# Kernel tuning notes

Hardware: AMD Instinct MI355X
Metric: run time of the kernel (lower is better)

Reference implementation:

```python
import jax, jax.numpy as jnp
import numpy as np

EPS = 1e-5
POW = 0.5

def _eig_fun(X, fn):
    # symmetric matrix function via eigendecomposition: V f(diag) V^T
    w, V = jnp.linalg.eigh(X)
    return jnp.einsum('...ij,...j,...kj->...ik', V, fn(w), V)

def sym_pow(X, p):
    return _eig_fun(X, lambda w: jnp.power(w, p))

def sym_log(X):
    return _eig_fun(X, jnp.log)

def sym_exp(X):
    return _eig_fun(X, jnp.exp)

def exp_at(T, G):
    # Riemannian exp of tangent T at base point G (affine-invariant metric)
    Gh = sym_pow(G, 0.5)
    Gnh = sym_pow(G, -0.5)
    return Gh @ sym_exp(Gnh @ T @ Gnh) @ Gh

def bary_geom(X, n_iter=1):
    # Karcher/geodesic mean of batch of SPD matrices X: (B, n, n)
    # init at arithmetic mean, n_iter Karcher flow steps
    G = jnp.mean(X, axis=0)
    for _ in range(n_iter):
        Gh = sym_pow(G, 0.5)
        Gnh = sym_pow(G, -0.5)
        T = jnp.mean(sym_log(Gnh @ X @ Gnh), axis=0)
        G = Gh @ sym_exp(T) @ Gh
    return G

def setup_inputs() -> dict:
    key = jax.random.key(0)
    N, h, n = 256, 16, 64
    k1, k2, k3 = jax.random.split(key, 3)
    A = jax.random.normal(k1, (N, h, n, n), dtype=jnp.float32)
    # well-conditioned SPD inputs with distinct eigenvalues
    X = A @ jnp.swapaxes(A, -1, -2) / n + 0.5 * jnp.eye(n, dtype=jnp.float32)
    Bw = jax.random.normal(k2, (n, n), dtype=jnp.float32) * 0.1
    weight = sym_exp(0.5 * (Bw + Bw.T))  # SPD parameter near identity
    Bm = jax.random.normal(k3, (n, n), dtype=jnp.float32) * 0.1
    M = sym_exp(0.5 * (Bm + Bm.T))       # SPD deformation parameter
    shift = jnp.ones((1,), dtype=jnp.float32)
    return {"X": X, "weight": weight, "M": M, "shift": shift}

def reference(X, weight, M, shift):
    N, h, n, _ = X.shape
    Xb = X.reshape(N * h, n, n)
    Xp = sym_pow(Xb, POW)                  # PowerEig(X, po)
    Mnh = sym_pow(M, -0.5)
    Mh = sym_pow(M, 0.5)
    Xc = Mnh @ Xp @ Mnh                    # CongrG(., M, 'neg')
    Wp = sym_pow(weight, POW)              # PowerEig(weight, po)
    Wc = Mnh @ Wp @ Mnh                    # CongrG1(weight, M, 'neg')

    mean = bary_geom(Xc)                   # BaryGeom (training path)
    mnh = sym_pow(mean, -0.5)
    # pal1(mean, LogG(Xc, mean)) = PT of Riemannian log to identity
    T = sym_log(mnh @ Xc @ mnh)            # (N*h, n, n) tangent at I
    # cal_var: mean squared Riemannian distance to the mean
    var = jnp.mean(jnp.sum(T * T, axis=(-2, -1)))
    T = T * (shift[0] / jnp.sqrt(var + EPS))  # scale1
    Wh = sym_pow(weight, 0.5)
    S = Wh @ T @ Wh                        # pal2(weight, LogG1(.))
    Y = exp_at(S, Wc)                      # ExpG(., weight_deformed)
    Y = Mh @ Y @ Mh                        # CongrG(., M, 'pos')
    Y = sym_pow(Y, 1.0 / POW)              # PowerEig(., 1/po)
    return Y.reshape(N, h, n, n)
```

## Files before the change

### kernel.cpp

```cpp
#include <hip/hip_runtime.h>
#include <math.h>

#define PITCH 72
#define NP 68
#define SW_BATCH 12
#define SW_SMALL 10
#define NPART 32
#define EPS2_ROT 1e-12f

#define OFF_ACCG 0
#define OFF_ACCT (NPART*4096)
#define OFF_BASE (2*NPART*4096)
#define SL_MNH  (OFF_BASE + 0*4096)
#define SL_MH   (OFF_BASE + 1*4096)
#define SL_WH   (OFF_BASE + 2*4096)
#define SL_P    (OFF_BASE + 3*4096)
#define SL_Q    (OFF_BASE + 4*4096)
#define SL_GH   (OFF_BASE + 5*4096)
#define SL_GNH  (OFF_BASE + 6*4096)
#define SL_MNH2 (OFF_BASE + 7*4096)
#define SL_WCH  (OFF_BASE + 8*4096)
#define OFF_VAR (OFF_BASE + 9*4096)
#define SL_SC   (OFF_BASE + 9*4096 + 1)

struct __align__(16) F4 { float v[4]; };

struct __align__(16) Smem {
  float S0[64*PITCH];
  float S1[64*PITCH];
  float w2[64];
  float wc[64];
  float nrm[64];
  float red[256];
  int flag;
};

__device__ __forceinline__ void g2s(float* dst, const float* __restrict__ src) {
  int t = threadIdx.x;
#pragma unroll
  for (int i = 0; i < 4; ++i) {
    int e4 = t + (i << 8);
    F4 vv = *(const F4*)&src[e4 * 4];
    *(F4*)&dst[(e4 >> 4) * PITCH + (e4 & 15) * 4] = vv;
  }
  __syncthreads();
}
__device__ __forceinline__ void s2g(float* __restrict__ dst, const float* src) {
  int t = threadIdx.x;
#pragma unroll
  for (int i = 0; i < 4; ++i) {
    int e4 = t + (i << 8);
    F4 vv = *(const F4*)&src[(e4 >> 4) * PITCH + (e4 & 15) * 4];
    *(F4*)&dst[e4 * 4] = vv;
  }
  __syncthreads();
}

template<int MODE>
__device__ void mmX(Smem& sm) {
  int t = threadIdx.x;
  int R0 = t >> 4;
  int J = (t & 15) * 4;
  float acc[4][4] = {};
  for (int kb = 0; kb < 64; kb += 4) {
    F4 a4[4], b4[4];
#pragma unroll
    for (int i = 0; i < 4; ++i) {
      const float* L = (MODE == 0) ? sm.S1 : sm.S0;
      a4[i] = *(const F4*)&L[(R0 + 16 * i) * PITCH + kb];
    }
#pragma unroll
    for (int kk = 0; kk < 4; ++kk) {
      const float* Rp = (MODE == 0) ? sm.S0 : sm.S1;
      b4[kk] = *(const F4*)&Rp[(kb + kk) * PITCH + J];
    }
#pragma unroll
    for (int i = 0; i < 4; ++i)
#pragma unroll
      for (int kk = 0; kk < 4; ++kk)
#pragma unroll
        for (int m = 0; m < 4; ++m)
          acc[i][m] = fmaf(a4[i].v[kk], b4[kk].v[m], acc[i][m]);
  }
  __syncthreads();
#pragma unroll
  for (int i = 0; i < 4; ++i) {
    F4 o;
#pragma unroll
    for (int m = 0; m < 4; ++m) o.v[m] = acc[i][m];
    *(F4*)&sm.S0[(R0 + 16 * i) * PITCH + J] = o;
  }
  __syncthreads();
}

__device__ void reconT(Smem& sm) {
  __syncthreads();
  int t = threadIdx.x;
  int R0 = t >> 4;
  int J = (t & 15) * 4;
  float acc[4][4] = {};
  for (int k = 0; k < 64; ++k) {
    float w = sm.wc[k];
    float a[4];
#pragma unroll
    for (int i = 0; i < 4; ++i) a[i] = w * sm.S0[k * PITCH + R0 + 16 * i];
    F4 b = *(const F4*)&sm.S0[k * PITCH + J];
#pragma unroll
    for (int i = 0; i < 4; ++i)
#pragma unroll
      for (int m = 0; m < 4; ++m) acc[i][m] = fmaf(a[i], b.v[m], acc[i][m]);
  }
#pragma unroll
  for (int i = 0; i < 4; ++i) {
    F4 o;
#pragma unroll
    for (int m = 0; m < 4; ++m) o.v[m] = acc[i][m];
    *(F4*)&sm.S1[(R0 + 16 * i) * PITCH + J] = o;
  }
  __syncthreads();
}

__device__ float frob2(Smem& sm) {
  int t = threadIdx.x;
  float s = 0.f;
#pragma unroll
  for (int i = 0; i < 4; ++i) {
    int e4 = t + (i << 8);
    F4 vv = *(const F4*)&sm.S0[(e4 >> 4) * PITCH + (e4 & 15) * 4];
#pragma unroll
    for (int m = 0; m < 4; ++m) s = fmaf(vv.v[m], vv.v[m], s);
  }
  sm.red[t] = s;
  __syncthreads();
  for (int o = 128; o; o >>= 1) { if (t < o) sm.red[t] += sm.red[t + o]; __syncthreads(); }
  float f = sm.red[0];
  __syncthreads();
  return f;
}

__device__ void hestenes(Smem& sm, int sweeps) {
  const int t = threadIdx.x;
  const int g = t >> 3;
  const int u = t & 7;
  float* A = sm.S0;
  {
    float sa = 0.f, sb = 0.f;
#pragma unroll
    for (int i = 0; i < 8; ++i) {
      float va = A[g * PITCH + u + 8 * i];
      float vb = A[(g + 32) * PITCH + u + 8 * i];
      sa = fmaf(va, va, sa); sb = fmaf(vb, vb, sb);
    }
    sa += __shfl_xor(sa, 1); sa += __shfl_xor(sa, 2); sa += __shfl_xor(sa, 4);
    sb += __shfl_xor(sb, 1); sb += __shfl_xor(sb, 2); sb += __shfl_xor(sb, 4);
    if (u == 0) { sm.nrm[g] = sa; sm.nrm[g + 32] = sb; }
    if (t == 0) sm.flag = 0;
  }
  __syncthreads();

  for (int s = 0; s < sweeps; ++s) {
    for (int r = 0; r < 63; ++r) {
      int p, q;
      if (g == 0) { p = 63; q = r; }
      else {
        int a = r + g;      if (a >= 63) a -= 63;
        int b = r + 63 - g; if (b >= 63) b -= 63;
        p = a; q = b;
      }
      const int bp = p * PITCH + u, bq = q * PITCH + u;
      float cp[8], cq[8];
#pragma unroll
      for (int i = 0; i < 8; ++i) { cp[i] = A[bp + 8 * i]; cq[i] = A[bq + 8 * i]; }
      float d = 0.f;
#pragma unroll
      for (int i = 0; i < 8; ++i) d = fmaf(cp[i], cq[i], d);
      d += __shfl_xor(d, 1); d += __shfl_xor(d, 2); d += __shfl_xor(d, 4);
      float dpp = sm.nrm[p], dqq = sm.nrm[q];
      if (d * d > EPS2_ROT * (dpp * dqq)) {
        float tau = (dqq - dpp) * (0.5f * __builtin_amdgcn_rcpf(d));
        float tt = __builtin_amdgcn_rcpf(fabsf(tau) +
                                         __builtin_amdgcn_sqrtf(fmaf(tau, tau, 1.f)));
        if (tau < 0.f) tt = -tt;
        float c = __builtin_amdgcn_rsqf(fmaf(tt, tt, 1.f));
        float s_ = tt * c;
#pragma unroll
        for (int i = 0; i < 8; ++i) {
          A[bp + 8 * i] = c * cp[i] - s_ * cq[i];
          A[bq + 8 * i] = s_ * cp[i] + c * cq[i];
        }
        if (u == 0) {
          float td = tt * d;
          sm.nrm[p] = dpp - td;
          sm.nrm[q] = dqq + td;
          sm.flag = 1;
        }
      }
      __syncthreads();
    }
    int f = sm.flag;
    __syncthreads();
    if (f == 0) break;
    if (t == 0) sm.flag = 0;
    __syncthreads();
  }

  {
    float sa = 0.f, sb = 0.f;
#pragma unroll
    for (int i = 0; i < 8; ++i) {
      float va = A[g * PITCH + u + 8 * i];
      float vb = A[(g + 32) * PITCH + u + 8 * i];
      sa = fmaf(va, va, sa); sb = fmaf(vb, vb, sb);
    }
    sa += __shfl_xor(sa, 1); sa += __shfl_xor(sa, 2); sa += __shfl_xor(sa, 4);
    sb += __shfl_xor(sb, 1); sb += __shfl_xor(sb, 2); sb += __shfl_xor(sb, 4);
    if (u == 0) { sm.w2[g] = sa; sm.w2[g + 32] = sb; }
  }
  __syncthreads();
}

struct __align__(16) SmemK {
  float A[64*NP];
  float Bop[64*NP];
  float wc[64];
  float red[256];
};
struct __align__(16) SmemK4 {
  float A[64*NP];
  float P[64*NP];
  float Q[64*NP];
  float wc[64];
  float red[256];
};

__device__ __forceinline__ void g2s68(float* dst, const float* __restrict__ src) {
  int t = threadIdx.x;
#pragma unroll
  for (int i = 0; i < 4; ++i) {
    int e4 = t + (i << 8);
    F4 vv = *(const F4*)&src[e4 * 4];
    *(F4*)&dst[(e4 >> 4) * NP + (e4 & 15) * 4] = vv;
  }
  __syncthreads();
}
__device__ __forceinline__ void g2s68s(float* dst, const float* __restrict__ src, float sc) {
  int t = threadIdx.x;
#pragma unroll
  for (int i = 0; i < 4; ++i) {
    int e4 = t + (i << 8);
    F4 vv = *(const F4*)&src[e4 * 4];
#pragma unroll
    for (int m = 0; m < 4; ++m) vv.v[m] *= sc;
    *(F4*)&dst[(e4 >> 4) * NP + (e4 & 15) * 4] = vv;
  }
  __syncthreads();
}

template<int MODE>
__device__ void mm68(float* A, const float* Bo) {
  int t = threadIdx.x;
  int R0 = t >> 4;
  if (MODE == 2) {
    int J0 = t & 15;
    float acc[4][4] = {};
    for (int kb = 0; kb < 64; kb += 4) {
      F4 a4[4];
#pragma unroll
      for (int i = 0; i < 4; ++i) a4[i] = *(const F4*)&A[(R0 + 16 * i) * NP + kb];
#pragma unroll
      for (int kk = 0; kk < 4; ++kk) {
        float b[4];
#pragma unroll
        for (int m = 0; m < 4; ++m) b[m] = Bo[(J0 + 16 * m) * NP + kb + kk];
#pragma unroll
        for (int i = 0; i < 4; ++i)
#pragma unroll
          for (int m = 0; m < 4; ++m) acc[i][m] = fmaf(a4[i].v[kk], b[m], acc[i][m]);
      }
    }
    __syncthreads();
#pragma unroll
    for (int i = 0; i < 4; ++i)
#pragma unroll
      for (int m = 0; m < 4; ++m)
        A[(R0 + 16 * i) * NP + J0 + 16 * m] = acc[i][m];
    __syncthreads();
  } else {
    int J = (t & 15) * 4;
    float acc[4][4] = {};
    for (int kb = 0; kb < 64; kb += 4) {
      F4 a4[4], b4[4];
#pragma unroll
      for (int i = 0; i < 4; ++i) {
        const float* L = (MODE == 0) ? Bo : A;
        a4[i] = *(const F4*)&L[(R0 + 16 * i) * NP + kb];
      }
#pragma unroll
      for (int kk = 0; kk < 4; ++kk) {
        const float* Rp = (MODE == 0) ? A : Bo;
        b4[kk] = *(const F4*)&Rp[(kb + kk) * NP + J];
      }
#pragma unroll
      for (int i = 0; i < 4; ++i)
#pragma unroll
        for (int kk = 0; kk < 4; ++kk)
#pragma unroll
          for (int m = 0; m < 4; ++m)
            acc[i][m] = fmaf(a4[i].v[kk], b4[kk].v[m], acc[i][m]);
    }
    __syncthreads();
#pragma unroll
    for (int i = 0; i < 4; ++i) {
      F4 o;
#pragma unroll
      for (int m = 0; m < 4; ++m) o.v[m] = acc[i][m];
      *(F4*)&A[(R0 + 16 * i) * NP + J] = o;
    }
    __syncthreads();
  }
}

__device__ float frob68(const float* A, float* red) {
  int t = threadIdx.x;
  float s = 0.f;
#pragma unroll
  for (int i = 0; i < 4; ++i) {
    int e4 = t + (i << 8);
    F4 vv = *(const F4*)&A[(e4 >> 4) * NP + (e4 & 15) * 4];
#pragma unroll
    for (int m = 0; m < 4; ++m) s = fmaf(vv.v[m], vv.v[m], s);
  }
  red[t] = s;
  __syncthreads();
  for (int o = 128; o; o >>= 1) { if (t < o) red[t] += red[t + o]; __syncthreads(); }
  float f = red[0];
  __syncthreads();
  return f;
}

__device__ void msq_store(const float* Z, float* __restrict__ gout) {
  int t = threadIdx.x;
  int R0 = t >> 4;
  int J = (t & 15) * 4;
  float acc[4][4] = {};
  for (int kb = 0; kb < 64; kb += 4) {
    F4 a4[4], b4[4];
#pragma unroll
    for (int i = 0; i < 4; ++i) a4[i] = *(const F4*)&Z[(R0 + 16 * i) * NP + kb];
#pragma unroll
    for (int kk = 0; kk < 4; ++kk) b4[kk] = *(const F4*)&Z[(kb + kk) * NP + J];
#pragma unroll
    for (int i = 0; i < 4; ++i)
#pragma unroll
      for (int kk = 0; kk < 4; ++kk)
#pragma unroll
        for (int m = 0; m < 4; ++m)
          acc[i][m] = fmaf(a4[i].v[kk], b4[kk].v[m], acc[i][m]);
  }
#pragma unroll
  for (int i = 0; i < 4; ++i) {
    F4 o;
#pragma unroll
    for (int m = 0; m < 4; ++m) o.v[m] = acc[i][m];
    *(F4*)&gout[(R0 + 16 * i) * 64 + J] = o;
  }
}

__device__ __forceinline__ void hestenes_reg(float (&own)[64], float& w2out, int sweeps) {
  const int lane = threadIdx.x & 63;
  float nrm = 0.f;
#pragma unroll
  for (int i = 0; i < 64; ++i) nrm = fmaf(own[i], own[i], nrm);

  for (int s = 0; s < sweeps; ++s) {
    bool any = false;
    for (int m = 1; m < 64; ++m) {
      float pv[64];
#pragma unroll
      for (int i = 0; i < 64; ++i) pv[i] = __shfl_xor(own[i], m);
      float d0 = 0.f, d1 = 0.f, d2 = 0.f, d3 = 0.f;
#pragma unroll
      for (int i = 0; i < 64; i += 4) {
        d0 = fmaf(own[i + 0], pv[i + 0], d0);
        d1 = fmaf(own[i + 1], pv[i + 1], d1);
        d2 = fmaf(own[i + 2], pv[i + 2], d2);
        d3 = fmaf(own[i + 3], pv[i + 3], d3);
      }
      float d = (d0 + d1) + (d2 + d3);
      float pn = __shfl_xor(nrm, m);
      if (d * d > EPS2_ROT * (nrm * pn)) {
        any = true;
        bool lo = lane < (lane ^ m);
        float dpp = lo ? nrm : pn;
        float dqq = lo ? pn : nrm;
        float tau = (dqq - dpp) * (0.5f * __builtin_amdgcn_rcpf(d));
        float tt = __builtin_amdgcn_rcpf(fabsf(tau) +
                                         __builtin_amdgcn_sqrtf(fmaf(tau, tau, 1.f)));
        if (tau < 0.f) tt = -tt;
        float c = __builtin_amdgcn_rsqf(fmaf(tt, tt, 1.f));
        float s_ = tt * c;
        float sg = lo ? -s_ : s_;
#pragma unroll
        for (int i = 0; i < 64; ++i) own[i] = fmaf(sg, pv[i], c * own[i]);
        float td = tt * d;
        nrm += lo ? -td : td;
      }
    }
    if (!__any((int)any)) break;
  }
  float w = 0.f;
#pragma unroll
  for (int i = 0; i < 64; ++i) w = fmaf(own[i], own[i], w);
  w2out = w;
}


__global__ __launch_bounds__(256) void kzero(float* ws) {
  int i = blockIdx.x * 256 + threadIdx.x;
  if (i < OFF_BASE) ws[i] = 0.f;
  if (i == 0) ws[OFF_VAR] = 0.f;
}

__global__ __launch_bounds__(256, 4) void kprep(const float* __restrict__ weight,
                                                const float* __restrict__ M,
                                                float* ws) {
  __shared__ Smem sm;
  int t = threadIdx.x;
  g2s(sm.S0, M);
  hestenes(sm, SW_SMALL);
  if (t < 64) sm.wc[t] = powf(fmaxf(sm.w2[t], 1e-12f), -1.25f);
  reconT(sm); s2g(ws + SL_MNH, sm.S1);
  if (t < 64) sm.wc[t] = powf(fmaxf(sm.w2[t], 1e-12f), -0.75f);
  reconT(sm); s2g(ws + SL_MH, sm.S1);

  g2s(sm.S0, weight);
  hestenes(sm, SW_SMALL);
  if (t < 64) sm.wc[t] = powf(fmaxf(sm.w2[t], 1e-12f), -0.75f);
  reconT(sm); s2g(ws + SL_WH, sm.S1);

  g2s(sm.S0, ws + SL_MNH);
  mmX<1>(sm);
  g2s(sm.S1, ws + SL_MNH);
  mmX<1>(sm);
  hestenes(sm, SW_SMALL);
  if (t < 64) sm.wc[t] = powf(fmaxf(sm.w2[t], 1e-12f), -0.75f);
  reconT(sm); s2g(ws + SL_WCH, sm.S1);
  if (t < 64) sm.wc[t] = powf(fmaxf(sm.w2[t], 1e-12f), -1.25f);
  reconT(sm);
  g2s(sm.S0, ws + SL_WH);
  mmX<0>(sm);
  s2g(ws + SL_P, sm.S0);
  g2s(sm.S0, ws + SL_WCH);
  g2s(sm.S1, ws + SL_MH);
  mmX<0>(sm);
  s2g(ws + SL_Q, sm.S0);
}

__global__ __launch_bounds__(256, 1) void k1(const float* __restrict__ X,
                                             float* __restrict__ out, float* ws) {
  __shared__ SmemK sm;
  int t = threadIdx.x;
  int w = t >> 6, lane = t & 63;
  size_t b = blockIdx.x;
  g2s68(sm.Bop, ws + SL_MNH);

  float own[64]; float w2;
  {
    const float* Xm = X + (b * 4 + w) * 4096 + (size_t)lane * 64;
#pragma unroll
    for (int j = 0; j < 16; ++j) {
      F4 r = *(const F4*)&Xm[4 * j];
      own[4 * j + 0] = r.v[0]; own[4 * j + 1] = r.v[1];
      own[4 * j + 2] = r.v[2]; own[4 * j + 3] = r.v[3];
    }
  }
  hestenes_reg(own, w2, SW_BATCH);
  __syncthreads();

  int R0 = t >> 4, J = (t & 15) * 4;
  for (int m = 0; m < 4; ++m) {
    if (w == m) {
#pragma unroll
      for (int j = 0; j < 16; ++j) {
        F4 o = {{own[4 * j], own[4 * j + 1], own[4 * j + 2], own[4 * j + 3]}};
        *(F4*)&sm.A[lane * NP + 4 * j] = o;
      }
      sm.wc[lane] = powf(fmaxf(w2, 1e-12f), -0.75f);
    }
    __syncthreads();
    mm68<1>(sm.A, sm.Bop);
    float acc[4][4] = {};
    for (int k = 0; k < 64; ++k) {
      float wck = sm.wc[k];
      float a[4];
#pragma unroll
      for (int i = 0; i < 4; ++i) a[i] = wck * sm.A[k * NP + R0 + 16 * i];
      F4 bb = *(const F4*)&sm.A[k * NP + J];
#pragma unroll
      for (int i = 0; i < 4; ++i)
#pragma unroll
        for (int mc = 0; mc < 4; ++mc) acc[i][mc] = fmaf(a[i], bb.v[mc], acc[i][mc]);
    }
    float* Xc = out + (b * 4 + m) * 4096;
    float* accp = ws + OFF_ACCG + (size_t)((b * 4 + m) & (NPART - 1)) * 4096;
#pragma unroll
    for (int i = 0; i < 4; ++i) {
      F4 o;
#pragma unroll
      for (int mc = 0; mc < 4; ++mc) o.v[mc] = acc[i][mc];
      int base = (R0 + 16 * i) * 64 + J;
      *(F4*)&Xc[base] = o;
#pragma unroll
      for (int mc = 0; mc < 4; ++mc) atomicAdd(accp + base + mc, o.v[mc]);
    }
    __syncthreads();
  }
}

__global__ __launch_bounds__(256, 4) void ksmall2(float* ws, float invB) {
  __shared__ Smem sm;
  int t = threadIdx.x;
#pragma unroll
  for (int i = 0; i < 4; ++i) {
    int e4 = t + (i << 8);
    F4 sum = {{0.f, 0.f, 0.f, 0.f}};
    for (int p = 0; p < NPART; ++p) {
      F4 vv = *(const F4*)&ws[OFF_ACCG + p * 4096 + e4 * 4];
#pragma unroll
      for (int m = 0; m < 4; ++m) sum.v[m] += vv.v[m];
    }
#pragma unroll
    for (int m = 0; m < 4; ++m) sum.v[m] *= invB;
    *(F4*)&sm.S0[(e4 >> 4) * PITCH + (e4 & 15) * 4] = sum;
  }
  __syncthreads();
  hestenes(sm, SW_SMALL);
  if (t < 64) sm.wc[t] = powf(fmaxf(sm.w2[t], 1e-12f), -0.75f);
  reconT(sm); s2g(ws + SL_GH, sm.S1);
  if (t < 64) sm.wc[t] = powf(fmaxf(sm.w2[t], 1e-12f), -1.25f);
  reconT(sm); s2g(ws + SL_GNH, sm.S1);
}

__global__ __launch_bounds__(256, 1) void k2(const float* __restrict__ XcBuf, float* ws) {
  __shared__ SmemK sm;
  int t = threadIdx.x;
  int w = t >> 6, lane = t & 63;
  size_t b = blockIdx.x;
  g2s68(sm.Bop, ws + SL_GNH);

  float own[64]; float w2;
  for (int m = 0; m < 4; ++m) {
    g2s68(sm.A, XcBuf + (b * 4 + m) * 4096);
    mm68<1>(sm.A, sm.Bop);
    mm68<0>(sm.A, sm.Bop);
    if (w == m) {
#pragma unroll
      for (int i = 0; i < 64; ++i) own[i] = sm.A[i * NP + lane];
    }
    __syncthreads();
  }
  hestenes_reg(own, w2, SW_BATCH);
  __syncthreads();

  int R0 = t >> 4, J = (t & 15) * 4;
  for (int m = 0; m < 4; ++m) {
    if (w == m) {
#pragma unroll
      for (int j = 0; j < 16; ++j) {
        F4 o = {{own[4 * j], own[4 * j + 1], own[4 * j + 2], own[4 * j + 3]}};
        *(F4*)&sm.A[lane * NP + 4 * j] = o;
      }
      float s2 = fmaxf(w2, 1e-12f);
      sm.wc[lane] = 0.5f * logf(s2) / s2;
    }
    __syncthreads();
    float acc[4][4] = {};
    for (int k = 0; k < 64; ++k) {
      float wck = sm.wc[k];
      float a[4];
#pragma unroll
      for (int i = 0; i < 4; ++i) a[i] = wck * sm.A[k * NP + R0 + 16 * i];
      F4 bb = *(const F4*)&sm.A[k * NP + J];
#pragma unroll
      for (int i = 0; i < 4; ++i)
#pragma unroll
        for (int mc = 0; mc < 4; ++mc) acc[i][mc] = fmaf(a[i], bb.v[mc], acc[i][mc]);
    }
    float* accp = ws + OFF_ACCT + (size_t)((b * 4 + m) & (NPART - 1)) * 4096;
#pragma unroll
    for (int i = 0; i < 4; ++i) {
      int base = (R0 + 16 * i) * 64 + J;
#pragma unroll
      for (int mc = 0; mc < 4; ++mc) atomicAdd(accp + base + mc, acc[i][mc]);
    }
    __syncthreads();
  }
}

__global__ __launch_bounds__(256, 4) void ksmall3(float* ws, float invB) {
  __shared__ Smem sm;
  int t = threadIdx.x;
#pragma unroll
  for (int i = 0; i < 4; ++i) {
    int e4 = t + (i << 8);
    F4 sum = {{0.f, 0.f, 0.f, 0.f}};
    for (int p = 0; p < NPART; ++p) {
      F4 vv = *(const F4*)&ws[OFF_ACCT + p * 4096 + e4 * 4];
#pragma unroll
      for (int m = 0; m < 4; ++m) sum.v[m] += vv.v[m];
    }
#pragma unroll
    for (int m = 0; m < 4; ++m) sum.v[m] *= invB;
    *(F4*)&sm.S0[(e4 >> 4) * PITCH + (e4 & 15) * 4] = sum;
  }
  __syncthreads();
  float mu = sqrtf(frob2(sm)) + 1e-3f;
  if (t < 64) sm.S0[t * PITCH + t] += mu;
  __syncthreads();
  hestenes(sm, SW_SMALL);
  if (t < 64) {
    float s2 = fmaxf(sm.w2[t], 1e-12f);
    sm.wc[t] = expf(sqrtf(s2) - mu) / s2;
  }
  reconT(sm);
  g2s(sm.S0, ws + SL_GH);
  mmX<1>(sm);
  g2s(sm.S1, ws + SL_GH);
  mmX<1>(sm);
  hestenes(sm, SW_SMALL);
  if (t < 64) sm.wc[t] = powf(fmaxf(sm.w2[t], 1e-12f), -1.25f);
  reconT(sm); s2g(ws + SL_MNH2, sm.S1);
}

__global__ __launch_bounds__(256, 1) void k3(float* __restrict__ buf, float* ws) {
  __shared__ SmemK sm;
  int t = threadIdx.x;
  int w = t >> 6, lane = t & 63;
  size_t b = blockIdx.x;
  g2s68(sm.Bop, ws + SL_MNH2);

  float own[64]; float w2;
  for (int m = 0; m < 4; ++m) {
    g2s68(sm.A, buf + (b * 4 + m) * 4096);
    mm68<1>(sm.A, sm.Bop);
    mm68<0>(sm.A, sm.Bop);
    if (w == m) {
#pragma unroll
      for (int i = 0; i < 64; ++i) own[i] = sm.A[i * NP + lane];
    }
    __syncthreads();
  }
  hestenes_reg(own, w2, SW_BATCH);
  __syncthreads();

  int R0 = t >> 4, J = (t & 15) * 4;
  for (int m = 0; m < 4; ++m) {
    if (w == m) {
#pragma unroll
      for (int j = 0; j < 16; ++j) {
        F4 o = {{own[4 * j], own[4 * j + 1], own[4 * j + 2], own[4 * j + 3]}};
        *(F4*)&sm.A[lane * NP + 4 * j] = o;
      }
      float s2 = fmaxf(w2, 1e-12f);
      sm.wc[lane] = 0.5f * logf(s2) / s2;
    }
    __syncthreads();
    float acc[4][4] = {};
    for (int k = 0; k < 64; ++k) {
      float wck = sm.wc[k];
      float a[4];
#pragma unroll
      for (int i = 0; i < 4; ++i) a[i] = wck * sm.A[k * NP + R0 + 16 * i];
      F4 bb = *(const F4*)&sm.A[k * NP + J];
#pragma unroll
      for (int i = 0; i < 4; ++i)
#pragma unroll
        for (int mc = 0; mc < 4; ++mc) acc[i][mc] = fmaf(a[i], bb.v[mc], acc[i][mc]);
    }
    float* Tg = buf + (b * 4 + m) * 4096;
    float ssq = 0.f;
#pragma unroll
    for (int i = 0; i < 4; ++i) {
      F4 o;
#pragma unroll
      for (int mc = 0; mc < 4; ++mc) o.v[mc] = acc[i][mc];
      int base = (R0 + 16 * i) * 64 + J;
      *(F4*)&Tg[base] = o;
#pragma unroll
      for (int mc = 0; mc < 4; ++mc) ssq = fmaf(o.v[mc], o.v[mc], ssq);
    }
    sm.red[t] = ssq;
    __syncthreads();
    for (int o = 128; o; o >>= 1) { if (t < o) sm.red[t] += sm.red[t + o]; __syncthreads(); }
    if (t == 0) atomicAdd(ws + OFF_VAR, sm.red[0]);
    __syncthreads();
  }
}

__global__ void kscale(float* ws, const float* __restrict__ shift, float invB) {
  if (threadIdx.x == 0 && blockIdx.x == 0) {
    float var = ws[OFF_VAR] * invB;
    ws[SL_SC] = shift[0] / sqrtf(var + 1e-5f);
  }
}

__global__ __launch_bounds__(256, 1) void k4(float* __restrict__ buf, float* ws) {
  __shared__ SmemK4 sm;
  int t = threadIdx.x;
  int w = t >> 6, lane = t & 63;
  size_t b = blockIdx.x;
  float sc = ws[SL_SC];
  g2s68(sm.P, ws + SL_P);
  g2s68(sm.Q, ws + SL_Q);

  float own[64]; float w2; float muw = 0.f;
  for (int m = 0; m < 4; ++m) {
    g2s68s(sm.A, buf + (b * 4 + m) * 4096, sc);
    mm68<0>(sm.A, sm.P);
    mm68<2>(sm.A, sm.P);
    float f = frob68(sm.A, sm.red);
    if (w == m) {
      muw = sqrtf(f) + 1e-3f;
#pragma unroll
      for (int i = 0; i < 64; ++i) {
        float v = sm.A[i * NP + lane];
        own[i] = v + ((i == lane) ? muw : 0.f);
      }
    }
    __syncthreads();
  }
  hestenes_reg(own, w2, SW_BATCH);
  __syncthreads();

  int R0 = t >> 4, J = (t & 15) * 4;
  for (int m = 0; m < 4; ++m) {
    if (w == m) {
#pragma unroll
      for (int j = 0; j < 16; ++j) {
        F4 o = {{own[4 * j], own[4 * j + 1], own[4 * j + 2], own[4 * j + 3]}};
        *(F4*)&sm.A[lane * NP + 4 * j] = o;
      }
      float s2 = fmaxf(w2, 1e-12f);
      sm.wc[lane] = expf(sqrtf(s2) - muw) / s2;
    }
    __syncthreads();
    mm68<2>(sm.A, sm.Q);
    float acc[4][4] = {};
    for (int k = 0; k < 64; ++k) {
      float wck = sm.wc[k];
      float a[4];
#pragma unroll
      for (int i = 0; i < 4; ++i) a[i] = wck * sm.A[k * NP + R0 + 16 * i];
      F4 bb = *(const F4*)&sm.A[k * NP + J];
#pragma unroll
      for (int i = 0; i < 4; ++i)
#pragma unroll
        for (int mc = 0; mc < 4; ++mc) acc[i][mc] = fmaf(a[i], bb.v[mc], acc[i][mc]);
    }
#pragma unroll
    for (int i = 0; i < 4; ++i) {
      F4 o;
#pragma unroll
      for (int mc = 0; mc < 4; ++mc) o.v[mc] = acc[i][mc];
      *(F4*)&sm.P[(R0 + 16 * i) * NP + J] = o;
    }
    __syncthreads();
    msq_store(sm.P, buf + (b * 4 + m) * 4096);
    __syncthreads();
  }
}

extern "C" void kernel_launch(void* const* d_in, const int* in_sizes, int n_in,
                              void* d_out, int out_size, void* d_ws, size_t ws_size,
                              hipStream_t stream) {
  const float* X      = (const float*)d_in[0];
  const float* weight = (const float*)d_in[1];
  const float* M      = (const float*)d_in[2];
  const float* shift  = (const float*)d_in[3];
  float* out = (float*)d_out;
  float* ws  = (float*)d_ws;
  int B = in_sizes[0] / 4096;
  float invB = 1.f / (float)B;
  int G = B / 4;

  hipLaunchKernelGGL(kzero,   dim3(OFF_BASE / 256), dim3(256), 0, stream, ws);
  hipLaunchKernelGGL(kprep,   dim3(1), dim3(256), 0, stream, weight, M, ws);
  hipLaunchKernelGGL(k1,      dim3(G), dim3(256), 0, stream, X, out, ws);
  hipLaunchKernelGGL(ksmall2, dim3(1), dim3(256), 0, stream, ws, invB);
  hipLaunchKernelGGL(k2,      dim3(G), dim3(256), 0, stream, out, ws);
  hipLaunchKernelGGL(ksmall3, dim3(1), dim3(256), 0, stream, ws, invB);
  hipLaunchKernelGGL(k3,      dim3(G), dim3(256), 0, stream, out, ws);
  hipLaunchKernelGGL(kscale,  dim3(1), dim3(64), 0, stream, ws, shift, invB);
  hipLaunchKernelGGL(k4,      dim3(G), dim3(256), 0, stream, out, ws);
}
```

Before: 8.990 ms.

## Use register Hestenes for small eigensolves and bpermute-batched shuffles

Replaces the shared-memory round-robin Hestenes Jacobi used by the single-matrix kernels with the register-resident per-wave variant, run by one wave per matrix. Inside hestenes_reg, the 64 shuffles per pair step become explicit ds_bpermute instructions followed by one wait and a schedule barrier, so the LDS permutes can be issued together. All kernels switch to an attribute allowing 1-2 waves per EU, which gives the compiler more registers for the 64-float arrays. The aim is to cut barrier-heavy serial work in the small kernels and shuffle latency in the batched ones, at the risk of idling three waves in the small kernels and changing occupancy.

New measurement: 9.408 ms. +4.7%, slower.

```diff
diff --git a/kernel.cpp b/kernel.cpp
--- a/kernel.cpp
+++ b/kernel.cpp
@@ -7,6 +7,8 @@
 #define SW_SMALL 10
 #define NPART 32
 #define EPS2_ROT 1e-12f
+
+#define KATTR __attribute__((amdgpu_flat_work_group_size(256, 256), amdgpu_waves_per_eu(1, 2)))
 
 #define OFF_ACCG 0
 #define OFF_ACCT (NPART*4096)
@@ -30,9 +32,7 @@
   float S1[64*PITCH];
   float w2[64];
   float wc[64];
-  float nrm[64];
   float red[256];
-  int flag;
 };
 
 __device__ __forceinline__ void g2s(float* dst, const float* __restrict__ src) {
@@ -138,234 +138,6 @@
   return f;
 }
 
-__device__ void hestenes(Smem& sm, int sweeps) {
-  const int t = threadIdx.x;
-  const int g = t >> 3;
-  const int u = t & 7;
-  float* A = sm.S0;
-  {
-    float sa = 0.f, sb = 0.f;
-#pragma unroll
-    for (int i = 0; i < 8; ++i) {
-      float va = A[g * PITCH + u + 8 * i];
-      float vb = A[(g + 32) * PITCH + u + 8 * i];
-      sa = fmaf(va, va, sa); sb = fmaf(vb, vb, sb);
-    }
-    sa += __shfl_xor(sa, 1); sa += __shfl_xor(sa, 2); sa += __shfl_xor(sa, 4);
-    sb += __shfl_xor(sb, 1); sb += __shfl_xor(sb, 2); sb += __shfl_xor(sb, 4);
-    if (u == 0) { sm.nrm[g] = sa; sm.nrm[g + 32] = sb; }
-    if (t == 0) sm.flag = 0;
-  }
-  __syncthreads();
-
-  for (int s = 0; s < sweeps; ++s) {
-    for (int r = 0; r < 63; ++r) {
-      int p, q;
-      if (g == 0) { p = 63; q = r; }
-      else {
-        int a = r + g;      if (a >= 63) a -= 63;
-        int b = r + 63 - g; if (b >= 63) b -= 63;
-        p = a; q = b;
-      }
-      const int bp = p * PITCH + u, bq = q * PITCH + u;
-      float cp[8], cq[8];
-#pragma unroll
-      for (int i = 0; i < 8; ++i) { cp[i] = A[bp + 8 * i]; cq[i] = A[bq + 8 * i]; }
-      float d = 0.f;
-#pragma unroll
-      for (int i = 0; i < 8; ++i) d = fmaf(cp[i], cq[i], d);
-      d += __shfl_xor(d, 1); d += __shfl_xor(d, 2); d += __shfl_xor(d, 4);
-      float dpp = sm.nrm[p], dqq = sm.nrm[q];
-      if (d * d > EPS2_ROT * (dpp * dqq)) {
-        float tau = (dqq - dpp) * (0.5f * __builtin_amdgcn_rcpf(d));
-        float tt = __builtin_amdgcn_rcpf(fabsf(tau) +
-                                         __builtin_amdgcn_sqrtf(fmaf(tau, tau, 1.f)));
-        if (tau < 0.f) tt = -tt;
-        float c = __builtin_amdgcn_rsqf(fmaf(tt, tt, 1.f));
-        float s_ = tt * c;
-#pragma unroll
-        for (int i = 0; i < 8; ++i) {
-          A[bp + 8 * i] = c * cp[i] - s_ * cq[i];
-          A[bq + 8 * i] = s_ * cp[i] + c * cq[i];
-        }
-        if (u == 0) {
-          float td = tt * d;
-          sm.nrm[p] = dpp - td;
-          sm.nrm[q] = dqq + td;
-          sm.flag = 1;
-        }
-      }
-      __syncthreads();
-    }
-    int f = sm.flag;
-    __syncthreads();
-    if (f == 0) break;
-    if (t == 0) sm.flag = 0;
-    __syncthreads();
-  }
-
-  {
-    float sa = 0.f, sb = 0.f;
-#pragma unroll
-    for (int i = 0; i < 8; ++i) {
-      float va = A[g * PITCH + u + 8 * i];
-      float vb = A[(g + 32) * PITCH + u + 8 * i];
-      sa = fmaf(va, va, sa); sb = fmaf(vb, vb, sb);
-    }
-    sa += __shfl_xor(sa, 1); sa += __shfl_xor(sa, 2); sa += __shfl_xor(sa, 4);
-    sb += __shfl_xor(sb, 1); sb += __shfl_xor(sb, 2); sb += __shfl_xor(sb, 4);
-    if (u == 0) { sm.w2[g] = sa; sm.w2[g + 32] = sb; }
-  }
-  __syncthreads();
-}
-
-struct __align__(16) SmemK {
-  float A[64*NP];
-  float Bop[64*NP];
-  float wc[64];
-  float red[256];
-};
-struct __align__(16) SmemK4 {
-  float A[64*NP];
-  float P[64*NP];
-  float Q[64*NP];
-  float wc[64];
-  float red[256];
-};
-
-__device__ __forceinline__ void g2s68(float* dst, const float* __restrict__ src) {
-  int t = threadIdx.x;
-#pragma unroll
-  for (int i = 0; i < 4; ++i) {
-    int e4 = t + (i << 8);
-    F4 vv = *(const F4*)&src[e4 * 4];
-    *(F4*)&dst[(e4 >> 4) * NP + (e4 & 15) * 4] = vv;
-  }
-  __syncthreads();
-}
-__device__ __forceinline__ void g2s68s(float* dst, const float* __restrict__ src, float sc) {
-  int t = threadIdx.x;
-#pragma unroll
-  for (int i = 0; i < 4; ++i) {
-    int e4 = t + (i << 8);
-    F4 vv = *(const F4*)&src[e4 * 4];
-#pragma unroll
-    for (int m = 0; m < 4; ++m) vv.v[m] *= sc;
-    *(F4*)&dst[(e4 >> 4) * NP + (e4 & 15) * 4] = vv;
-  }
-  __syncthreads();
-}
-
-template<int MODE>
-__device__ void mm68(float* A, const float* Bo) {
-  int t = threadIdx.x;
-  int R0 = t >> 4;
-  if (MODE == 2) {
-    int J0 = t & 15;
-    float acc[4][4] = {};
-    for (int kb = 0; kb < 64; kb += 4) {
-      F4 a4[4];
-#pragma unroll
-      for (int i = 0; i < 4; ++i) a4[i] = *(const F4*)&A[(R0 + 16 * i) * NP + kb];
-#pragma unroll
-      for (int kk = 0; kk < 4; ++kk) {
-        float b[4];
-#pragma unroll
-        for (int m = 0; m < 4; ++m) b[m] = Bo[(J0 + 16 * m) * NP + kb + kk];
-#pragma unroll
-        for (int i = 0; i < 4; ++i)
-#pragma unroll
-          for (int m = 0; m < 4; ++m) acc[i][m] = fmaf(a4[i].v[kk], b[m], acc[i][m]);
-      }
-    }
-    __syncthreads();
-#pragma unroll
-    for (int i = 0; i < 4; ++i)
-#pragma unroll
-      for (int m = 0; m < 4; ++m)
-        A[(R0 + 16 * i) * NP + J0 + 16 * m] = acc[i][m];
-    __syncthreads();
-  } else {
-    int J = (t & 15) * 4;
-    float acc[4][4] = {};
-    for (int kb = 0; kb < 64; kb += 4) {
-      F4 a4[4], b4[4];
-#pragma unroll
-      for (int i = 0; i < 4; ++i) {
-        const float* L = (MODE == 0) ? Bo : A;
-        a4[i] = *(const F4*)&L[(R0 + 16 * i) * NP + kb];
-      }
-#pragma unroll
-      for (int kk = 0; kk < 4; ++kk) {
-        const float* Rp = (MODE == 0) ? A : Bo;
-        b4[kk] = *(const F4*)&Rp[(kb + kk) * NP + J];
-      }
-#pragma unroll
-      for (int i = 0; i < 4; ++i)
-#pragma unroll
-        for (int kk = 0; kk < 4; ++kk)
-#pragma unroll
-          for (int m = 0; m < 4; ++m)
-            acc[i][m] = fmaf(a4[i].v[kk], b4[kk].v[m], acc[i][m]);
-    }
-    __syncthreads();
-#pragma unroll
-    for (int i = 0; i < 4; ++i) {
-      F4 o;
-#pragma unroll
-      for (int m = 0; m < 4; ++m) o.v[m] = acc[i][m];
-      *(F4*)&A[(R0 + 16 * i) * NP + J] = o;
-    }
-    __syncthreads();
-  }
-}
-
-__device__ float frob68(const float* A, float* red) {
-  int t = threadIdx.x;
-  float s = 0.f;
-#pragma unroll
-  for (int i = 0; i < 4; ++i) {
-    int e4 = t + (i << 8);
-    F4 vv = *(const F4*)&A[(e4 >> 4) * NP + (e4 & 15) * 4];
-#pragma unroll
-    for (int m = 0; m < 4; ++m) s = fmaf(vv.v[m], vv.v[m], s);
-  }
-  red[t] = s;
-  __syncthreads();
-  for (int o = 128; o; o >>= 1) { if (t < o) red[t] += red[t + o]; __syncthreads(); }
-  float f = red[0];
-  __syncthreads();
-  return f;
-}
-
-__device__ void msq_store(const float* Z, float* __restrict__ gout) {
-  int t = threadIdx.x;
-  int R0 = t >> 4;
-  int J = (t & 15) * 4;
-  float acc[4][4] = {};
-  for (int kb = 0; kb < 64; kb += 4) {
-    F4 a4[4], b4[4];
-#pragma unroll
-    for (int i = 0; i < 4; ++i) a4[i] = *(const F4*)&Z[(R0 + 16 * i) * NP + kb];
-#pragma unroll
-    for (int kk = 0; kk < 4; ++kk) b4[kk] = *(const F4*)&Z[(kb + kk) * NP + J];
-#pragma unroll
-    for (int i = 0; i < 4; ++i)
-#pragma unroll
-      for (int kk = 0; kk < 4; ++kk)
-#pragma unroll
-        for (int m = 0; m < 4; ++m)
-          acc[i][m] = fmaf(a4[i].v[kk], b4[kk].v[m], acc[i][m]);
-  }
-#pragma unroll
-  for (int i = 0; i < 4; ++i) {
-    F4 o;
-#pragma unroll
-    for (int m = 0; m < 4; ++m) o.v[m] = acc[i][m];
-    *(F4*)&gout[(R0 + 16 * i) * 64 + J] = o;
-  }
-}
-
 __device__ __forceinline__ void hestenes_reg(float (&own)[64], float& w2out, int sweeps) {
   const int lane = threadIdx.x & 63;
   float nrm = 0.f;
@@ -375,9 +147,14 @@
   for (int s = 0; s < sweeps; ++s) {
     bool any = false;
     for (int m = 1; m < 64; ++m) {
+      const int paddr = ((lane ^ m) << 2);
       float pv[64];
 #pragma unroll
-      for (int i = 0; i < 64; ++i) pv[i] = __shfl_xor(own[i], m);
+      for (int i = 0; i < 64; ++i)
+        asm volatile("ds_bpermute_b32 %0, %1, %2"
+                     : "=v"(pv[i]) : "v"(paddr), "v"(own[i]));
+      asm volatile("s_waitcnt lgkmcnt(0)" ::: "memory");
+      __builtin_amdgcn_sched_barrier(0);
       float d0 = 0.f, d1 = 0.f, d2 = 0.f, d3 = 0.f;
 #pragma unroll
       for (int i = 0; i < 64; i += 4) {
@@ -414,6 +191,168 @@
   w2out = w;
 }
 
+__device__ void hestenes_small(Smem& sm, int sweeps) {
+  const int t = threadIdx.x;
+  if (t < 64) {
+    float own[64];
+#pragma unroll
+    for (int i = 0; i < 64; ++i) own[i] = sm.S0[t * PITCH + i];
+    float w2;
+    hestenes_reg(own, w2, sweeps);
+#pragma unroll
+    for (int i = 0; i < 64; ++i) sm.S0[t * PITCH + i] = own[i];
+    sm.w2[t] = w2;
+  }
+  __syncthreads();
+}
+
+struct __align__(16) SmemK {
+  float A[64*NP];
+  float Bop[64*NP];
+  float wc[64];
+  float red[256];
+};
+struct __align__(16) SmemK4 {
+  float A[64*NP];
+  float P[64*NP];
+  float Q[64*NP];
+  float wc[64];
+  float red[256];
+};
+
+__device__ __forceinline__ void g2s68(float* dst, const float* __restrict__ src) {
+  int t = threadIdx.x;
+#pragma unroll
+  for (int i = 0; i < 4; ++i) {
+    int e4 = t + (i << 8);
+    F4 vv = *(const F4*)&src[e4 * 4];
+    *(F4*)&dst[(e4 >> 4) * NP + (e4 & 15) * 4] = vv;
+  }
+  __syncthreads();
+}
+__device__ __forceinline__ void g2s68s(float* dst, const float* __restrict__ src, float sc) {
+  int t = threadIdx.x;
+#pragma unroll
+  for (int i = 0; i < 4; ++i) {
+    int e4 = t + (i << 8);
+    F4 vv = *(const F4*)&src[e4 * 4];
+#pragma unroll
+    for (int m = 0; m < 4; ++m) vv.v[m] *= sc;
+    *(F4*)&dst[(e4 >> 4) * NP + (e4 & 15) * 4] = vv;
+  }
+  __syncthreads();
+}
+
+template<int MODE>
+__device__ void mm68(float* A, const float* Bo) {
+  int t = threadIdx.x;
+  int R0 = t >> 4;
+  if (MODE == 2) {
+    int J0 = t & 15;
+    float acc[4][4] = {};
+    for (int kb = 0; kb < 64; kb += 4) {
+      F4 a4[4];
+#pragma unroll
+      for (int i = 0; i < 4; ++i) a4[i] = *(const F4*)&A[(R0 + 16 * i) * NP + kb];
+#pragma unroll
+      for (int kk = 0; kk < 4; ++kk) {
+        float b[4];
+#pragma unroll
+        for (int m = 0; m < 4; ++m) b[m] = Bo[(J0 + 16 * m) * NP + kb + kk];
+#pragma unroll
+        for (int i = 0; i < 4; ++i)
+#pragma unroll
+          for (int m = 0; m < 4; ++m) acc[i][m] = fmaf(a4[i].v[kk], b[m], acc[i][m]);
+      }
+    }
+    __syncthreads();
+#pragma unroll
+    for (int i = 0; i < 4; ++i)
+#pragma unroll
+      for (int m = 0; m < 4; ++m)
+        A[(R0 + 16 * i) * NP + J0 + 16 * m] = acc[i][m];
+    __syncthreads();
+  } else {
+    int J = (t & 15) * 4;
+    float acc[4][4] = {};
+    for (int kb = 0; kb < 64; kb += 4) {
+      F4 a4[4], b4[4];
+#pragma unroll
+      for (int i = 0; i < 4; ++i) {
+        const float* L = (MODE == 0) ? Bo : A;
+        a4[i] = *(const F4*)&L[(R0 + 16 * i) * NP + kb];
+      }
+#pragma unroll
+      for (int kk = 0; kk < 4; ++kk) {
+        const float* Rp = (MODE == 0) ? A : Bo;
+        b4[kk] = *(const F4*)&Rp[(kb + kk) * NP + J];
+      }
+#pragma unroll
+      for (int i = 0; i < 4; ++i)
+#pragma unroll
+        for (int kk = 0; kk < 4; ++kk)
+#pragma unroll
+          for (int m = 0; m < 4; ++m)
+            acc[i][m] = fmaf(a4[i].v[kk], b4[kk].v[m], acc[i][m]);
+    }
+    __syncthreads();
+#pragma unroll
+    for (int i = 0; i < 4; ++i) {
+      F4 o;
+#pragma unroll
+      for (int m = 0; m < 4; ++m) o.v[m] = acc[i][m];
+      *(F4*)&A[(R0 + 16 * i) * NP + J] = o;
+    }
+    __syncthreads();
+  }
+}
+
+__device__ float frob68(const float* A, float* red) {
+  int t = threadIdx.x;
+  float s = 0.f;
+#pragma unroll
+  for (int i = 0; i < 4; ++i) {
+    int e4 = t + (i << 8);
+    F4 vv = *(const F4*)&A[(e4 >> 4) * NP + (e4 & 15) * 4];
+#pragma unroll
+    for (int m = 0; m < 4; ++m) s = fmaf(vv.v[m], vv.v[m], s);
+  }
+  red[t] = s;
+  __syncthreads();
+  for (int o = 128; o; o >>= 1) { if (t < o) red[t] += red[t + o]; __syncthreads(); }
+  float f = red[0];
+  __syncthreads();
+  return f;
+}
+
+__device__ void msq_store(const float* Z, float* __restrict__ gout) {
+  int t = threadIdx.x;
+  int R0 = t >> 4;
+  int J = (t & 15) * 4;
+  float acc[4][4] = {};
+  for (int kb = 0; kb < 64; kb += 4) {
+    F4 a4[4], b4[4];
+#pragma unroll
+    for (int i = 0; i < 4; ++i) a4[i] = *(const F4*)&Z[(R0 + 16 * i) * NP + kb];
+#pragma unroll
+    for (int kk = 0; kk < 4; ++kk) b4[kk] = *(const F4*)&Z[(kb + kk) * NP + J];
+#pragma unroll
+    for (int i = 0; i < 4; ++i)
+#pragma unroll
+      for (int kk = 0; kk < 4; ++kk)
+#pragma unroll
+        for (int m = 0; m < 4; ++m)
+          acc[i][m] = fmaf(a4[i].v[kk], b4[kk].v[m], acc[i][m]);
+  }
+#pragma unroll
+  for (int i = 0; i < 4; ++i) {
+    F4 o;
+#pragma unroll
+    for (int m = 0; m < 4; ++m) o.v[m] = acc[i][m];
+    *(F4*)&gout[(R0 + 16 * i) * 64 + J] = o;
+  }
+}
+
 
 __global__ __launch_bounds__(256) void kzero(float* ws) {
   int i = blockIdx.x * 256 + threadIdx.x;
@@ -421,20 +360,20 @@
   if (i == 0) ws[OFF_VAR] = 0.f;
 }
 
-__global__ __launch_bounds__(256, 4) void kprep(const float* __restrict__ weight,
-                                                const float* __restrict__ M,
-                                                float* ws) {
+__global__ KATTR void kprep(const float* __restrict__ weight,
+                            const float* __restrict__ M,
+                            float* ws) {
   __shared__ Smem sm;
   int t = threadIdx.x;
   g2s(sm.S0, M);
-  hestenes(sm, SW_SMALL);
+  hestenes_small(sm, SW_SMALL);
   if (t < 64) sm.wc[t] = powf(fmaxf(sm.w2[t], 1e-12f), -1.25f);
   reconT(sm); s2g(ws + SL_MNH, sm.S1);
   if (t < 64) sm.wc[t] = powf(fmaxf(sm.w2[t], 1e-12f), -0.75f);
   reconT(sm); s2g(ws + SL_MH, sm.S1);
 
   g2s(sm.S0, weight);
-  hestenes(sm, SW_SMALL);
+  hestenes_small(sm, SW_SMALL);
   if (t < 64) sm.wc[t] = powf(fmaxf(sm.w2[t], 1e-12f), -0.75f);
   reconT(sm); s2g(ws + SL_WH, sm.S1);
 
@@ -442,7 +381,7 @@
   mmX<1>(sm);
   g2s(sm.S1, ws + SL_MNH);
   mmX<1>(sm);
-  hestenes(sm, SW_SMALL);
+  hestenes_small(sm, SW_SMALL);
   if (t < 64) sm.wc[t] = powf(fmaxf(sm.w2[t], 1e-12f), -0.75f);
   reconT(sm); s2g(ws + SL_WCH, sm.S1);
   if (t < 64) sm.wc[t] = powf(fmaxf(sm.w2[t], 1e-12f), -1.25f);
@@ -456,8 +395,8 @@
   s2g(ws + SL_Q, sm.S0);
 }
 
-__global__ __launch_bounds__(256, 1) void k1(const float* __restrict__ X,
-                                             float* __restrict__ out, float* ws) {
+__global__ KATTR void k1(const float* __restrict__ X,
+                         float* __restrict__ out, float* ws) {
   __shared__ SmemK sm;
   int t = threadIdx.x;
   int w = t >> 6, lane = t & 63;
@@ -517,7 +456,7 @@
   }
 }
 
-__global__ __launch_bounds__(256, 4) void ksmall2(float* ws, float invB) {
+__global__ KATTR void ksmall2(float* ws, float invB) {
   __shared__ Smem sm;
   int t = threadIdx.x;
 #pragma unroll
@@ -534,14 +473,14 @@
     *(F4*)&sm.S0[(e4 >> 4) * PITCH + (e4 & 15) * 4] = sum;
   }
   __syncthreads();
-  hestenes(sm, SW_SMALL);
+  hestenes_small(sm, SW_SMALL);
   if (t < 64) sm.wc[t] = powf(fmaxf(sm.w2[t], 1e-12f), -0.75f);
   reconT(sm); s2g(ws + SL_GH, sm.S1);
   if (t < 64) sm.wc[t] = powf(fmaxf(sm.w2[t], 1e-12f), -1.25f);
   reconT(sm); s2g(ws + SL_GNH, sm.S1);
 }
 
-__global__ __launch_bounds__(256, 1) void k2(const float* __restrict__ XcBuf, float* ws) {
+__global__ KATTR void k2(const float* __restrict__ XcBuf, float* ws) {
   __shared__ SmemK sm;
   int t = threadIdx.x;
   int w = t >> 6, lane = t & 63;
@@ -597,7 +536,7 @@
   }
 }
 
-__global__ __launch_bounds__(256, 4) void ksmall3(float* ws, float invB) {
+__global__ KATTR void ksmall3(float* ws, float invB) {
   __shared__ Smem sm;
   int t = threadIdx.x;
 #pragma unroll
@@ -617,7 +556,7 @@
   float mu = sqrtf(frob2(sm)) + 1e-3f;
   if (t < 64) sm.S0[t * PITCH + t] += mu;
   __syncthreads();
-  hestenes(sm, SW_SMALL);
+  hestenes_small(sm, SW_SMALL);
   if (t < 64) {
     float s2 = fmaxf(sm.w2[t], 1e-12f);
     sm.wc[t] = expf(sqrtf(s2) - mu) / s2;
@@ -627,12 +566,12 @@
   mmX<1>(sm);
   g2s(sm.S1, ws + SL_GH);
   mmX<1>(sm);
-  hestenes(sm, SW_SMALL);
+  hestenes_small(sm, SW_SMALL);
   if (t < 64) sm.wc[t] = powf(fmaxf(sm.w2[t], 1e-12f), -1.25f);
   reconT(sm); s2g(ws + SL_MNH2, sm.S1);
 }
 
-__global__ __launch_bounds__(256, 1) void k3(float* __restrict__ buf, float* ws) {
+__global__ KATTR void k3(float* __restrict__ buf, float* ws) {
   __shared__ SmemK sm;
   int t = threadIdx.x;
   int w = t >> 6, lane = t & 63;
@@ -704,7 +643,7 @@
   }
 }
 
-__global__ __launch_bounds__(256, 1) void k4(float* __restrict__ buf, float* ws) {
+__global__ KATTR void k4(float* __restrict__ buf, float* ws) {
   __shared__ SmemK4 sm;
   int t = threadIdx.x;
   int w = t >> 6, lane = t & 63;
```
